# Kernel optimization log

Measured on AMD Instinct MI355X. Metric: run time of the kernel, lower is better.

The kernel has to match this reference:

```python
import jax, jax.numpy as jnp
import numpy as np
from jax.ops import segment_sum, segment_max

N, H, E, NEXP, K, L, HEADS, NM = 384, 768, 12288, 8, 2, 3, 4, 38
GAMMA, LAMBDA_SPD = 2.0, 0.5


def _ln(x, g, b, eps=1e-5):
    m = jnp.mean(x, -1, keepdims=True)
    v = jnp.mean((x - m) ** 2, -1, keepdims=True)
    return (x - m) / jnp.sqrt(v + eps) * g + b


def _gelu(x):
    return jax.nn.gelu(x, approximate=False)


def setup_inputs() -> dict:
    key = jax.random.key(0)
    ks = jax.random.split(key, 20)
    r = lambda i, sh: jax.random.normal(ks[i], sh, jnp.float32) * 0.02
    z = lambda sh: jnp.zeros(sh, jnp.float32)
    o = lambda sh: jnp.ones(sh, jnp.float32)
    return dict(
        feat_text=jax.random.normal(ks[0], (N, H), jnp.float32),
        feat_image=jax.random.normal(ks[1], (N, H), jnp.float32),
        spd_matrix=jax.random.uniform(ks[2], (N, N), dtype=jnp.float32),
        src=jax.random.randint(ks[3], (E,), 0, N, jnp.int32),
        dst=jax.random.randint(ks[4], (E,), 0, N, jnp.int32),
        mask_idx=jax.random.randint(ks[5], (NM,), 0, N, jnp.int32),
        mask_token=r(6, (H,)),
        gate_W=r(7, (H, NEXP)), gate_b=z((NEXP,)),
        exp_W1=r(8, (NEXP, H, H)), exp_b1=z((NEXP, H)),
        exp_g1=o((NEXP, H)), exp_be1=z((NEXP, H)),
        exp_W2=r(9, (NEXP, H, H)), exp_b2=z((NEXP, H)),
        gat_W=r(10, (L, H, HEADS * H)), gat_al=r(11, (L, HEADS, H)),
        gat_ar=r(12, (L, HEADS, H)), gat_b=z((L, HEADS * H)),
        dec_W1=r(13, (2, H, H)), dec_b1=z((2, H)),
        dec_g=o((2, H)), dec_be=z((2, H)),
        dec_W2=r(14, (2, H, H)), dec_b2=z((2, H)),
        spd_W1=r(15, (2 * H, H)), spd_b1=z((H,)),
        spd_g=o((H,)), spd_be=z((H,)),
        spd_W2=r(16, (H, 1)), spd_b2=z((1,)),
    )


def _forward(feat_text, feat_image, spd_matrix, mask_token, gate_W, gate_b,
             exp_W1, exp_b1, exp_g1, exp_be1, exp_W2, exp_b2,
             gat_W, gat_al, gat_ar, gat_b,
             dec_W1, dec_b1, dec_g, dec_be, dec_W2, dec_b2,
             spd_W1, spd_b1, spd_g, spd_be, spd_W2, spd_b2,
             src, dst, mask_idx):
    # mean of domain features, then mask-token replacement at fixed indices
    x = (feat_text + feat_image) * 0.5
    xm = x.at[mask_idx].set(mask_token)

    # --- MoE (all experts computed densely, top-2 gathered, as in source) ---
    gw = jax.nn.softmax(xm @ gate_W + gate_b, axis=-1)              # [N,NEXP]
    topw, topi = jax.lax.top_k(gw, K)
    topw = topw / jnp.sum(topw, -1, keepdims=True)
    eh = _gelu(_ln(jnp.einsum('nd,edh->neh', xm, exp_W1) + exp_b1, exp_g1, exp_be1))
    eo = jnp.einsum('neh,ehk->nek', eh, exp_W2) + exp_b2            # [N,NEXP,H]
    sel = jnp.take_along_axis(eo, topi[:, :, None], axis=1)          # [N,K,H]
    h = jnp.sum(sel * topw[:, :, None], axis=1)                      # [N,H]

    # --- stacked GATConv layers (DGL semantics), head-mean after each ---
    for l in range(L):
        f = (h @ gat_W[l]).reshape(N, HEADS, H)                      # [N,heads,H]
        el = jnp.sum(f * gat_al[l], -1)                              # [N,heads]
        er = jnp.sum(f * gat_ar[l], -1)
        e = jax.nn.leaky_relu(el[src] + er[dst], 0.2)                # [E,heads]
        emax = segment_max(e, dst, num_segments=N)
        emax = jnp.where(jnp.isfinite(emax), emax, 0.0)
        ex = jnp.exp(e - emax[dst])
        den = segment_sum(ex, dst, num_segments=N)
        alpha = ex / jnp.maximum(den[dst], 1e-9)                     # edge softmax by dst
        rst = segment_sum(alpha[:, :, None] * f[src], dst, num_segments=N)
        h = jnp.mean(rst + gat_b[l].reshape(HEADS, H), axis=1)       # [N,H]

    # --- domain reconstruction loss on masked nodes ---
    hm = h[mask_idx]
    feats = (feat_text, feat_image)
    recon = jnp.float32(0.0)
    for d in range(2):
        zz = _gelu(_ln(hm @ dec_W1[d] + dec_b1[d], dec_g[d], dec_be[d]))
        rec = zz @ dec_W2[d] + dec_b2[d]
        orig = feats[d][mask_idx]
        denom = jnp.maximum(jnp.linalg.norm(rec, axis=-1) * jnp.linalg.norm(orig, axis=-1), 1e-8)
        cos = jnp.sum(rec * orig, -1) / denom
        recon = recon + jnp.mean((1.0 - cos) ** GAMMA)

    # --- SPD loss over all N^2 pairs, vectorized ---
    # concat([h_i, h_j]) @ W1 == h_i @ W1[:H] + h_j @ W1[H:]  (exact decomposition)
    pa = h @ spd_W1[:H]                                              # [N,H]
    pb = h @ spd_W1[H:]                                              # [N,H]
    zp = _gelu(_ln(pa[:, None, :] + pb[None, :, :] + spd_b1, spd_g, spd_be))  # [N,N,H]
    pred = (zp @ spd_W2)[..., 0] + spd_b2[0]                         # [N,N]
    spd_loss = jnp.mean((pred - spd_matrix) ** 2)

    total = recon + LAMBDA_SPD * spd_loss
    return total, h


def reference(feat_text, feat_image, spd_matrix, src, dst, mask_idx, mask_token,
              gate_W, gate_b, exp_W1, exp_b1, exp_g1, exp_be1, exp_W2, exp_b2,
              gat_W, gat_al, gat_ar, gat_b,
              dec_W1, dec_b1, dec_g, dec_be, dec_W2, dec_b2,
              spd_W1, spd_b1, spd_g, spd_be, spd_W2, spd_b2):
    return _forward(feat_text, feat_image, spd_matrix, mask_token, gate_W, gate_b,
                    exp_W1, exp_b1, exp_g1, exp_be1, exp_W2, exp_b2,
                    gat_W, gat_al, gat_ar, gat_b,
                    dec_W1, dec_b1, dec_g, dec_be, dec_W2, dec_b2,
                    spd_W1, spd_b1, spd_g, spd_be, spd_W2, spd_b2,
                    src, dst, mask_idx)
```

## Files before the change

kernel.cpp:

```cpp
#include <hip/hip_runtime.h>
#include <hip/hip_bf16.h>
#include <math.h>

#define NN 384
#define HD 768
#define EE 12288
#define NCHUNK (EE / 256)
#define NEXPERT 8
#define TOPK 2
#define NLAYER 3
#define NHEADS 4
#define NMASK 38

typedef __attribute__((ext_vector_type(8))) short short8v;
typedef __attribute__((ext_vector_type(4))) float f32x4;
typedef __attribute__((ext_vector_type(2))) float f32x2;
typedef __attribute__((ext_vector_type(4))) int int4v;

__device__ __forceinline__ float gelu_f(float x) {
    return x * 0.5f * (1.f + erff(x * 0.70710678118654752440f));
}

__device__ __forceinline__ ushort f2bf(float x) {
    unsigned u = __float_as_uint(x);
    u += 0x7fffu + ((u >> 16) & 1u);
    return (ushort)(u >> 16);
}

__global__ __launch_bounds__(256) void k_xm_gate(const float* __restrict__ a,
        const float* __restrict__ b, const int* __restrict__ mask_idx,
        const float* __restrict__ mt, ushort* __restrict__ xm_bf,
        const float* __restrict__ gW, const float* __restrict__ gb,
        int* __restrict__ topi, float* __restrict__ topw) {
    int n = blockIdx.x, tid = threadIdx.x;
    __shared__ float xs[HD];
    __shared__ int ism;
    __shared__ float logits[NEXPERT];
    if (tid == 0) ism = 0;
    __syncthreads();
    if (tid < NMASK && mask_idx[tid] == n) ism = 1;
    __syncthreads();
#pragma unroll
    for (int r = 0; r < 3; r++) {
        int j = r * 256 + tid;
        float v = ism ? mt[j] : 0.5f * (a[(size_t)n * HD + j] + b[(size_t)n * HD + j]);
        xs[j] = v;
        xm_bf[(size_t)n * HD + j] = f2bf(v);
    }
// ... 23 lines not shown
        for (int e = 0; e < NEXPERT; e++) if (e != i0 && sm[e] > b1v) { b1v = sm[e]; i1 = e; }
        float ssum = b0 + b1v;
        topi[n * 2] = i0; topi[n * 2 + 1] = i1;
        topw[n * 2] = b0 / ssum; topw[n * 2 + 1] = b1v / ssum;
    }
}

__global__ __launch_bounds__(256) void k_transpose_all(
        const float* __restrict__ w1, const float* __restrict__ w2,
        const float* __restrict__ gw, const float* __restrict__ sw,
        const float* __restrict__ dw1, const float* __restrict__ dw2,
        ushort* __restrict__ o1, ushort* __restrict__ o2, ushort* __restrict__ og,
        ushort* __restrict__ os, ushort* __restrict__ od1, ushort* __restrict__ od2) {
    int b = blockIdx.x;
    const float* src; ushort* dst; int N, loc, tilesX;
    if (b < 4608)       { src = w1;  dst = o1;  N = HD;     loc = b;         tilesX = 24; }
    else if (b < 9216)  { src = w2;  dst = o2;  N = HD;     loc = b - 4608;  tilesX = 24; }
    else if (b < 16128) { src = gw;  dst = og;  N = 4 * HD; loc = b - 9216;  tilesX = 96; }
    else if (b < 17280) { src = sw;  dst = os;  N = HD;     loc = b - 16128; tilesX = 24; }
    else if (b < 18432) { src = dw1; dst = od1; N = HD;     loc = b - 17280; tilesX = 24; }
    else                { src = dw2; dst = od2; N = HD;     loc = b - 18432; tilesX = 24; }
    const int K = HD;
    int tilesPerZ = tilesX * 24;
    int z = loc / tilesPerZ;
    int rem = loc - z * tilesPerZ;
    int ty = rem / tilesX, tx = rem - ty * tilesX;
    const float* inz = src + (size_t)z * K * N;
    ushort* outz = dst + (size_t)z * K * N;
    int n0 = tx * 32, k0 = ty * 32;

    __shared__ float t[32][36];
    int r = threadIdx.x >> 3, c4 = (threadIdx.x & 7) * 4;
    float4 v = *reinterpret_cast<const float4*>(inz + (size_t)(k0 + r) * N + n0 + c4);
    t[r][c4] = v.x; t[r][c4 + 1] = v.y; t[r][c4 + 2] = v.z; t[r][c4 + 3] = v.w;
    __syncthreads();
    int orow = n0 + r;
    uint2 p;
    ushort b0 = f2bf(t[c4 + 0][r]);
    ushort b1 = f2bf(t[c4 + 1][r]);
    ushort b2 = f2bf(t[c4 + 2][r]);
    ushort b3 = f2bf(t[c4 + 3][r]);
    p.x = (unsigned)b0 | ((unsigned)b1 << 16);
    p.y = (unsigned)b2 | ((unsigned)b3 << 16);
    *reinterpret_cast<uint2*>(outz + (size_t)orow * K + k0 + c4) = p;
}

__global__ __launch_bounds__(256) void k_moe_meta(const int* __restrict__ topi,
        int* __restrict__ ecnt, int* __restrict__ estart, int* __restrict__ posArr,
        int* __restrict__ eofpos, int* __restrict__ rowlist, int* __restrict__ dec_rs) {
    __shared__ int ti[NN * TOPK];
    __shared__ int cnt[NEXPERT];
    __shared__ int est[NEXPERT + 1];
    int tid = threadIdx.x;
    if (tid < NEXPERT) cnt[tid] = 0;
    __syncthreads();
    for (int a = tid; a < NN * TOPK; a += 256) ti[a] = topi[a];
    __syncthreads();
    for (int a = tid; a < NN * TOPK; a += 256) atomicAdd(&cnt[ti[a]], 1);
    __syncthreads();
    if (tid == 0) {
        int s = 0;
        for (int e = 0; e < NEXPERT; e++) { est[e] = s; s += cnt[e]; }
        est[NEXPERT] = s;
        dec_rs[0] = 0; dec_rs[1] = NMASK;
    }
    __syncthreads();
    if (tid < NEXPERT) { ecnt[tid] = cnt[tid]; estart[tid] = est[tid]; }
    if (tid == 0) estart[NEXPERT] = est[NEXPERT];
    for (int a = tid; a < NN * TOPK; a += 256) {
        int e = ti[a]; int rank = 0;
        for (int a2 = 0; a2 < a; a2++) rank += (ti[a2] == e) ? 1 : 0;
        int p = est[e] + rank;
        posArr[a] = p; eofpos[p] = e; rowlist[p] = a >> 1;
    }
}

__global__ __launch_bounds__(256) void k_hist(const int* __restrict__ dst,
                                              int* __restrict__ counts) {
    __shared__ int h[NN];
    int c = blockIdx.x;
    for (int i = threadIdx.x; i < NN; i += 256) h[i] = 0;
    __syncthreads();
    atomicAdd(&h[dst[c * 256 + threadIdx.x]], 1);
    __syncthreads();
    for (int i = threadIdx.x; i < NN; i += 256) counts[c * NN + i] = h[i];
}

__global__ __launch_bounds__(NN) void k_scan_all(const int* __restrict__ counts,
        int* __restrict__ chunkbase, int* __restrict__ nstart) {
    __shared__ int tot[NN];
    int n = threadIdx.x;
    int s = 0;
    for (int c = 0; c < NCHUNK; c++) { chunkbase[c * NN + n] = s; s += counts[c * NN + n]; }
    tot[n] = s;
    __syncthreads();
    for (int off = 1; off < NN; off <<= 1) {
        int v = tot[n];
        int add = (n >= off) ? tot[n - off] : 0;
        __syncthreads();
        tot[n] = v + add;
        __syncthreads();
    }
    nstart[n + 1] = tot[n];
    if (n == 0) nstart[0] = 0;
}

__global__ __launch_bounds__(256) void k_rank2(const int* __restrict__ dst,
        const int* __restrict__ chunkbase, const int* __restrict__ nstart,
        int* __restrict__ esorted) {
    __shared__ int ds[256];
    int c = blockIdx.x;
    int e = c * 256 + threadIdx.x;
    int d = dst[e];
    ds[threadIdx.x] = d;
    __syncthreads();
    int r = 0;
    for (int i = 0; i < threadIdx.x; i++) r += (ds[i] == d) ? 1 : 0;
    esorted[nstart[d] + chunkbase[c * NN + d] + r] = e;
}

__device__ __forceinline__ short8v ldfrag(const ushort* s, int r, int kb) {
    int c = kb ^ (r & 7);
    return *reinterpret_cast<const short8v*>(s + r * 64 + c * 8);
}

__global__ __launch_bounds__(256) void k_mfma_gemm(
        const ushort* __restrict__ A, const ushort* __restrict__ Bt, float* __restrict__ C,
        int M, int K, int lda, int ldc, long strideBt, long strideC,
        const int* __restrict__ rowsA, const int* __restrict__ Ms,
        const int* __restrict__ rowStarts) {
    int z = blockIdx.z;
    int Meff = Ms ? Ms[z] : M;
    int row0 = blockIdx.y * 64;
    if (row0 >= Meff) return;
    int col0 = blockIdx.x * 64;
    int rowbase = rowStarts ? rowStarts[z] : 0;
    const ushort* Btz = Bt + (size_t)z * strideBt;
    float* Cz = C + (size_t)rowbase * ldc + (size_t)z * strideC;
    const int* rz = rowsA ? (rowsA + rowbase) : nullptr;

    __shared__ ushort Asm[64 * 64];
    __shared__ ushort Bsm[64 * 64];

    int tid = threadIdx.x;
    int w = tid >> 6, lane = tid & 63;
    int wr = w >> 1, wc = w & 1;
    int l15 = lane & 15, lq = lane >> 4;

    f32x4 acc[2][2];
#pragma unroll
    for (int i = 0; i < 2; i++)
#pragma unroll
        for (int j = 0; j < 2; j++) acc[i][j] = (f32x4){0.f, 0.f, 0.f, 0.f};

    for (int k0 = 0; k0 < K; k0 += 64) {
#pragma unroll
        for (int ii = 0; ii < 2; ii++) {
// ... 25 lines not shown
        }
        __syncthreads();
    }
#pragma unroll
    for (int ai = 0; ai < 2; ai++)
#pragma unroll
        for (int bi = 0; bi < 2; bi++) {
            int rbase = row0 + wr * 32 + ai * 16 + (lq << 2);
            int cc = col0 + wc * 32 + bi * 16 + l15;
#pragma unroll
            for (int r = 0; r < 4; r++) {
                int rr = rbase + r;
                if (rr < Meff) Cz[(size_t)rr * ldc + cc] = acc[ai][bi][r];
            }
        }
}

__global__ __launch_bounds__(256) void k_ln_gelu(const float* __restrict__ t1,
        ushort* __restrict__ ehb, const float* __restrict__ b1, const float* __restrict__ g,
        const float* __restrict__ be, const int* __restrict__ eofpos) {
    int row = blockIdx.x;
    int e = eofpos[row];
    int tid = threadIdx.x;
    __shared__ float rA[4], rB[4];
    float v[3]; float s1 = 0.f, s2 = 0.f;
#pragma unroll
    for (int r = 0; r < 3; r++) {
        int c = r * 256 + tid;
        float x = t1[(size_t)row * HD + c] + b1[e * HD + c];
        v[r] = x; s1 += x; s2 += x * x;
// ... 141 lines not shown
        }
        __syncthreads();
    }
#pragma unroll
    for (int r = 0; r < 3; r++) {
        int j = r * 256 + tid;
        float s = 0.f;
#pragma unroll
        for (int hd = 0; hd < NHEADS; hd++) s += acc[hd][r] + gb[hd * HD + j];
        float hv = 0.25f * s;
        hout[(size_t)n * HD + j] = hv;
        hb[(size_t)n * HD + j] = f2bf(hv);
    }
}

__global__ __launch_bounds__(256) void k_ln_gelu_dec(const float* __restrict__ t1,
        ushort* __restrict__ zzb, const float* __restrict__ b1, const float* __restrict__ g,
        const float* __restrict__ be) {
    int m = blockIdx.x, d = blockIdx.y;
    int row = d * NMASK + m;
    int tid = threadIdx.x;
    __shared__ float rA[4], rB[4];
    float v[3]; float s1 = 0.f, s2 = 0.f;
#pragma unroll
    for (int r = 0; r < 3; r++) {
        int c = r * 256 + tid;
        float x = t1[(size_t)row * HD + c] + b1[d * HD + c];
        v[r] = x; s1 += x; s2 += x * x;
    }
#pragma unroll
    for (int mm = 1; mm < 64; mm <<= 1) { s1 += __shfl_xor(s1, mm); s2 += __shfl_xor(s2, mm); }
    int wave = tid >> 6, lane = tid & 63;
    if (lane == 0) { rA[wave] = s1; rB[wave] = s2; }
    __syncthreads();
    float S1 = rA[0] + rA[1] + rA[2] + rA[3];
    float S2 = rB[0] + rB[1] + rB[2] + rB[3];
    float mean = S1 * (1.f / HD);
    float var = S2 * (1.f / HD) - mean * mean;
    float rstd = rsqrtf(var + 1e-5f);
#pragma unroll
    for (int r = 0; r < 3; r++) {
        int c = r * 256 + tid;
        float zn = (v[r] - mean) * rstd * g[d * HD + c] + be[d * HD + c];
        zzb[(size_t)row * HD + c] = f2bf(gelu_f(zn));
    }
}

__global__ __launch_bounds__(256) void k_cos(const float* __restrict__ rec,
        const float* __restrict__ b2, const int* __restrict__ mask_idx,
        const float* __restrict__ ft, const float* __restrict__ fi,
        float* __restrict__ rec_part) {
    int b = blockIdx.x;
    int d = b / NMASK, m = b % NMASK;
    int node = mask_idx[m];
    int tid = threadIdx.x;
    __shared__ float rA[4], rB[4], rC[4];
    const float* rrow = rec + (size_t)b * HD;
    const float* orig = (d == 0 ? ft : fi) + (size_t)node * HD;
    float pro = 0.f, prr = 0.f, poo = 0.f;
#pragma unroll
    for (int r = 0; r < 3; r++) {
        int c = r * 256 + tid;
        float rv = rrow[c] + b2[d * HD + c];
        float o = orig[c];
        pro += rv * o; prr += rv * rv; poo += o * o;
    }
#pragma unroll
    for (int mm = 1; mm < 64; mm <<= 1) {
        pro += __shfl_xor(pro, mm); prr += __shfl_xor(prr, mm); poo += __shfl_xor(poo, mm);
    }
    int wave = tid >> 6, lane = tid & 63;
    if (lane == 0) { rA[wave] = pro; rB[wave] = prr; rC[wave] = poo; }
    __syncthreads();
    if (tid == 0) {
        float P = rA[0] + rA[1] + rA[2] + rA[3];
        float R = rB[0] + rB[1] + rB[2] + rB[3];
        float O = rC[0] + rC[1] + rC[2] + rC[3];
        float denom = fmaxf(sqrtf(R) * sqrtf(O), 1e-8f);
        float cosv = P / denom;
        float t = 1.f - cosv;
        rec_part[b] = (t * t) * (1.f / (float)NMASK);
    }
}

__global__ __launch_bounds__(256) void k_spd_prep(float* __restrict__ pab,
        const float* __restrict__ b1, ushort* __restrict__ pp_bf,
        float* __restrict__ Svec, float* __restrict__ Qvec) {
    int r = blockIdx.x, tid = threadIdx.x;
    bool isA = r < NN;
    float* row = pab + (size_t)r * HD;
    __shared__ float rA[4], rB[4];
    float vv[3]; float s1 = 0.f, s2 = 0.f;
#pragma unroll
    for (int rr = 0; rr < 3; rr++) {
        int j = rr * 256 + tid;
        float v = row[j];
        if (isA) v += b1[j];
        vv[rr] = v; s1 += v; s2 += v * v;
    }
#pragma unroll
    for (int m = 1; m < 64; m <<= 1) { s1 += __shfl_xor(s1, m); s2 += __shfl_xor(s2, m); }
    int wave = tid >> 6, lane = tid & 63;
    if (lane == 0) { rA[wave] = s1; rB[wave] = s2; }
#pragma unroll
    for (int rr = 0; rr < 3; rr++) {
        int j = rr * 256 + tid;
        if (isA) row[j] = vv[rr];
        pp_bf[(size_t)r * HD + j] = f2bf(vv[rr]);
    }
    __syncthreads();
    if (tid == 0) {
        Svec[r] = rA[0] + rA[1] + rA[2] + rA[3];
        Qvec[r] = rB[0] + rB[1] + rB[2] + rB[3];
    }
}

#define GC1 2.3022085f
#define GC2 0.10294429f
__global__ __launch_bounds__(256) void k_spd2(const float* __restrict__ pab,
        const float* __restrict__ Svec, const float* __restrict__ Qvec,
        const float* __restrict__ cross, const float* __restrict__ g,
        const float* __restrict__ be, const float* __restrict__ w2,
        const float* __restrict__ b2, const float* __restrict__ spd,
        float* __restrict__ partials) {
    __shared__ float wsum[4];
    int i = blockIdx.x;
    int wave = threadIdx.x >> 6, lane = threadIdx.x & 63;
    const f32x2* paP = reinterpret_cast<const f32x2*>(pab + (size_t)i * HD);
    const f32x2* gP = reinterpret_cast<const f32x2*>(g);
    const f32x2* beP = reinterpret_cast<const f32x2*>(be);
    const f32x2* w2P = reinterpret_cast<const f32x2*>(w2);
    f32x2 pa2[6], g2[6], be2[6], w22[6];
#pragma unroll
    for (int r = 0; r < 6; r++) {
        int e = r * 64 + lane;
        pa2[r] = paP[e];
        g2[r] = gP[e];
        be2[r] = beP[e];
        w22[r] = w2P[e];
    }
    float Sa = Svec[i], Qa = Qvec[i];
    float bacc = 0.f;
    float b2v = b2[0];
    for (int j = blockIdx.y * 4 + wave; j < NN; j += 32) {
        const f32x2* pbj = reinterpret_cast<const f32x2*>(pab + (size_t)(NN + j) * HD);
        float mean = (Sa + Svec[NN + j]) * (1.f / HD);
        float ex2 = (Qa + Qvec[NN + j] + 2.f * cross[(size_t)i * NN + j]) * (1.f / HD);
        float var = ex2 - mean * mean;
        float rstd = rsqrtf(var + 1e-5f);
        f32x2 rstd2 = (f32x2){rstd, rstd};
        float nmr = -mean * rstd;
        f32x2 nmr2 = (f32x2){nmr, nmr};
        f32x2 dot2 = (f32x2){0.f, 0.f};
#pragma unroll
        for (int r = 0; r < 6; r++) {
            f32x2 z = pa2[r] + pbj[r * 64 + lane];
            f32x2 u = z * rstd2 + nmr2;
            f32x2 zn = u * g2[r] + be2[r];
            f32x2 t2 = zn * zn;
            f32x2 p = t2 * (f32x2){GC2, GC2} + (f32x2){GC1, GC1};
            f32x2 ua = zn * p;
            float e0 = __builtin_amdgcn_exp2f(-ua.x);
            float e1 = __builtin_amdgcn_exp2f(-ua.y);
            f32x2 rr = (f32x2){__builtin_amdgcn_rcpf(1.f + e0),
                               __builtin_amdgcn_rcpf(1.f + e1)};
            f32x2 gl = zn * rr;
            dot2 = gl * w22[r] + dot2;
        }
        float dot = dot2.x + dot2.y;
#pragma unroll
        for (int m = 1; m < 64; m <<= 1) dot += __shfl_xor(dot, m);
        if (lane == 0) {
            float d = (dot + b2v) - spd[(size_t)i * NN + j];
            bacc += d * d;
        }
    }
    if (lane == 0) wsum[wave] = bacc;
    __syncthreads();
    if (threadIdx.x == 0) partials[i * 8 + blockIdx.y] = wsum[0] + wsum[1] + wsum[2] + wsum[3];
}

__global__ __launch_bounds__(256) void k_out(const float* __restrict__ h,
        const float* __restrict__ rec_part, const float* __restrict__ spd_part,
        float* __restrict__ out) {
    if (blockIdx.x < NN * HD / 256) {
        int i = blockIdx.x * 256 + threadIdx.x;
        out[1 + i] = h[i];
        return;
    }
    __shared__ float rA[4], rB[4];
    int tid = threadIdx.x;
    float sp = 0.f, rc = 0.f;
    for (int t = tid; t < 8 * NN; t += 256) sp += spd_part[t];
    for (int t = tid; t < 2 * NMASK; t += 256) rc += rec_part[t];
#pragma unroll
    for (int m = 1; m < 64; m <<= 1) { sp += __shfl_xor(sp, m); rc += __shfl_xor(rc, m); }
    int wave = tid >> 6, lane = tid & 63;
    if (lane == 0) { rA[wave] = sp; rB[wave] = rc; }
    __syncthreads();
    if (tid == 0) {
        float SP = rA[0] + rA[1] + rA[2] + rA[3];
        float RC = rB[0] + rB[1] + rB[2] + rB[3];
        out[0] = RC + 0.5f * (SP * (1.f / ((float)NN * (float)NN)));
    }
}

extern "C" void kernel_launch(void* const* d_in, const int* in_sizes, int n_in,
                              void* d_out, int out_size, void* d_ws, size_t ws_size,
// ... 35 lines not shown
    size_t off = 0;
    auto alloc = [&](size_t nfl) { float* p = ws + off; off += (nfl + 3) & ~(size_t)3; return p; };
    float* hA   = alloc((size_t)NN * HD);
    float* hB   = alloc((size_t)NN * HD);
    float* t1   = alloc((size_t)NN * TOPK * HD);
    float* eo   = alloc((size_t)NN * TOPK * HD);
    float* fbuf = alloc((size_t)NN * NHEADS * HD);
    float* el   = alloc(NN * NHEADS);
    float* er   = alloc(NN * NHEADS);
    float* pab  = alloc((size_t)2 * NN * HD);
    float* cross = alloc((size_t)NN * NN);
    float* Svec = alloc(2 * NN);
    float* Qvec = alloc(2 * NN);
    float* topw = alloc(NN * TOPK);
    float* rec_part = alloc(2 * NMASK + 4);
    float* spd_part = alloc(8 * NN);
    int* topi    = (int*)alloc(NN * TOPK);
    int* ecnt    = (int*)alloc(16);
    int* estart  = (int*)alloc(16);
    int* posArr  = (int*)alloc(NN * TOPK);
    int* eofpos  = (int*)alloc(NN * TOPK);
    int* rowlist = (int*)alloc(NN * TOPK);
    int* dec_rs  = (int*)alloc(4);
    int* nstart  = (int*)alloc(NN + 4);
    int* esorted = (int*)alloc(EE);
    int* counts    = (int*)alloc((size_t)NCHUNK * NN);
    int* chunkbase = (int*)alloc((size_t)NCHUNK * NN);
    ushort* xm_bf  = (ushort*)alloc((size_t)NN * HD / 2);
    ushort* eh_bf  = (ushort*)alloc((size_t)NN * TOPK * HD / 2);
    ushort* hA_bf  = (ushort*)alloc((size_t)NN * HD / 2);
    ushort* hB_bf  = (ushort*)alloc((size_t)NN * HD / 2);
    ushort* pp_bf  = (ushort*)alloc((size_t)2 * NN * HD / 2);
    ushort* expW1t = (ushort*)alloc((size_t)NEXPERT * HD * HD / 2);
    ushort* expW2t = (ushort*)alloc((size_t)NEXPERT * HD * HD / 2);
    ushort* gatWt  = (ushort*)alloc((size_t)NLAYER * NHEADS * HD * HD / 2);
    ushort* spdW1t = (ushort*)alloc((size_t)2 * HD * HD / 2);
    ushort* decW1t = (ushort*)alloc((size_t)2 * HD * HD / 2);
    ushort* decW2t = (ushort*)alloc((size_t)2 * HD * HD / 2);

    k_transpose_all<<<dim3(19584), dim3(256), 0, stream>>>(
        exp_W1, exp_W2, gat_W, spd_W1, dec_W1, dec_W2,
        expW1t, expW2t, gatWt, spdW1t, decW1t, decW2t);

    k_xm_gate<<<dim3(NN), dim3(256), 0, stream>>>(
        feat_text, feat_image, mask_idx, mask_token, xm_bf, gate_W, gate_b, topi, topw);
    k_moe_meta<<<dim3(1), dim3(256), 0, stream>>>(topi, ecnt, estart, posArr, eofpos,
                                                  rowlist, dec_rs);

    k_hist<<<dim3(NCHUNK), dim3(256), 0, stream>>>(dst, counts);
    k_scan_all<<<dim3(1), dim3(NN), 0, stream>>>(counts, chunkbase, nstart);
    k_rank2<<<dim3(NCHUNK), dim3(256), 0, stream>>>(dst, chunkbase, nstart, esorted);

    k_mfma_gemm<<<dim3(HD / 64, 12, NEXPERT), dim3(256), 0, stream>>>(
        xm_bf, expW1t, t1, 0, HD, HD, HD, (long)HD * HD, 0, rowlist, ecnt, estart);
    k_ln_gelu<<<dim3(NN * TOPK), dim3(256), 0, stream>>>(t1, eh_bf, exp_b1, exp_g1, exp_be1, eofpos);
    k_mfma_gemm<<<dim3(HD / 64, 12, NEXPERT), dim3(256), 0, stream>>>(
        eh_bf, expW2t, eo, 0, HD, HD, HD, (long)HD * HD, 0, nullptr, ecnt, estart);
    k_combine_moe<<<dim3(NN), dim3(256), 0, stream>>>(eo, exp_b2, topi, topw, posArr, hA, hA_bf);

    float* hcur = hA; float* hnxt = hB;
    ushort* hcur_bf = hA_bf; ushort* hnxt_bf = hB_bf;
    for (int l = 0; l < NLAYER; l++) {
        k_mfma_gemm<<<dim3(NHEADS * HD / 64, NN / 64, 1), dim3(256), 0, stream>>>(
            hcur_bf, gatWt + (size_t)l * NHEADS * HD * HD, fbuf,
            NN, HD, HD, NHEADS * HD, 0, 0, nullptr, nullptr, nullptr);
        k_el_er<<<dim3(NN), dim3(256), 0, stream>>>(
            fbuf, gat_al + (size_t)l * NHEADS * HD, gat_ar + (size_t)l * NHEADS * HD, el, er);
        k_gat_agg<<<dim3(NN), dim3(256), 0, stream>>>(
            fbuf, el, er, src, esorted, nstart, gat_b + (size_t)l * NHEADS * HD, hnxt, hnxt_bf);
        float* t = hcur; hcur = hnxt; hnxt = t;
        ushort* tb = hcur_bf; hcur_bf = hnxt_bf; hnxt_bf = tb;
    }

    k_mfma_gemm<<<dim3(HD / 64, 1, 2), dim3(256), 0, stream>>>(
        hcur_bf, decW1t, t1, NMASK, HD, HD, HD, (long)HD * HD, (long)NMASK * HD,
        mask_idx, nullptr, nullptr);
    k_ln_gelu_dec<<<dim3(NMASK, 2), dim3(256), 0, stream>>>(t1, eh_bf, dec_b1, dec_g, dec_be);
    k_mfma_gemm<<<dim3(HD / 64, 1, 2), dim3(256), 0, stream>>>(
        eh_bf, decW2t, eo, NMASK, HD, HD, HD, (long)HD * HD, 0,
        nullptr, nullptr, dec_rs);
    k_cos<<<dim3(2 * NMASK), dim3(256), 0, stream>>>(
        eo, dec_b2, mask_idx, feat_text, feat_image, rec_part);

    k_mfma_gemm<<<dim3(HD / 64, NN / 64, 2), dim3(256), 0, stream>>>(
        hcur_bf, spdW1t, pab, NN, HD, HD, HD, (long)HD * HD, (long)NN * HD,
        nullptr, nullptr, nullptr);
    k_spd_prep<<<dim3(2 * NN), dim3(256), 0, stream>>>(pab, spd_b1, pp_bf, Svec, Qvec);
    k_mfma_gemm<<<dim3(NN / 64, NN / 64, 1), dim3(256), 0, stream>>>(
        pp_bf, pp_bf + (size_t)NN * HD, cross, NN, HD, HD, NN, 0, 0,
        nullptr, nullptr, nullptr);
    k_spd2<<<dim3(NN, 8), dim3(256), 0, stream>>>(
        pab, Svec, Qvec, cross, spd_g, spd_be, spd_W2, spd_b2, spd_matrix, spd_part);

    k_out<<<dim3(NN * HD / 256 + 1), dim3(256), 0, stream>>>(
        hcur, rec_part, spd_part, (float*)d_out);
}
```

Before: 364.8 us.

## Merge independent small kernels into combined launches and retile transpose and SPD loop

Folds the edge histogram into the gate kernel, the scan and MoE metadata into one launch, and pairs the independent decoder and SPD GEMMs into dual-GEMM launches indexed by blockIdx.z. The decoder LN/GELU is merged into the SPD prep, and the cosine loss is merged into the SPD loss kernel. The goal is fewer serialized launches and better GPU fill during the tail. The weight transpose now handles 64x32 tiles with 16-byte stores, and the SPD loop is restructured to process two columns per iteration with 32 partials per row. In exchange, the kernels become more branchy and some blocks in the merged grids exit early as idle.

```diff
diff --git a/kernel.cpp b/kernel.cpp
--- a/kernel.cpp
+++ b/kernel.cpp
@@ -27,11 +27,22 @@
     return (ushort)(u >> 16);
 }
 
-__global__ __launch_bounds__(256) void k_xm_gate(const float* __restrict__ a,
+__global__ __launch_bounds__(256) void k_xm_gate_hist(const float* __restrict__ a,
         const float* __restrict__ b, const int* __restrict__ mask_idx,
         const float* __restrict__ mt, ushort* __restrict__ xm_bf,
         const float* __restrict__ gW, const float* __restrict__ gb,
-        int* __restrict__ topi, float* __restrict__ topw) {
+        int* __restrict__ topi, float* __restrict__ topw,
+        const int* __restrict__ dst, int* __restrict__ counts) {
+    if (blockIdx.x >= NN) {
+        __shared__ int h[NN];
+        int c = blockIdx.x - NN;
+        for (int i = threadIdx.x; i < NN; i += 256) h[i] = 0;
+        __syncthreads();
+        atomicAdd(&h[dst[c * 256 + threadIdx.x]], 1);
+        __syncthreads();
+        for (int i = threadIdx.x; i < NN; i += 256) counts[c * NN + i] = h[i];
+        return;
+    }
     int n = blockIdx.x, tid = threadIdx.x;
     __shared__ float xs[HD];
     __shared__ int ism;
@@ -85,49 +96,75 @@
         ushort* __restrict__ os, ushort* __restrict__ od1, ushort* __restrict__ od2) {
     int b = blockIdx.x;
     const float* src; ushort* dst; int N, loc, tilesX;
-    if (b < 4608)       { src = w1;  dst = o1;  N = HD;     loc = b;         tilesX = 24; }
-    else if (b < 9216)  { src = w2;  dst = o2;  N = HD;     loc = b - 4608;  tilesX = 24; }
-    else if (b < 16128) { src = gw;  dst = og;  N = 4 * HD; loc = b - 9216;  tilesX = 96; }
-    else if (b < 17280) { src = sw;  dst = os;  N = HD;     loc = b - 16128; tilesX = 24; }
-    else if (b < 18432) { src = dw1; dst = od1; N = HD;     loc = b - 17280; tilesX = 24; }
-    else                { src = dw2; dst = od2; N = HD;     loc = b - 18432; tilesX = 24; }
+    if (b < 2304)      { src = w1;  dst = o1;  N = HD;     loc = b;        tilesX = 24; }
+    else if (b < 4608) { src = w2;  dst = o2;  N = HD;     loc = b - 2304; tilesX = 24; }
+    else if (b < 8064) { src = gw;  dst = og;  N = 4 * HD; loc = b - 4608; tilesX = 96; }
+    else if (b < 8640) { src = sw;  dst = os;  N = HD;     loc = b - 8064; tilesX = 24; }
+    else if (b < 9216) { src = dw1; dst = od1; N = HD;     loc = b - 8640; tilesX = 24; }
+    else               { src = dw2; dst = od2; N = HD;     loc = b - 9216; tilesX = 24; }
     const int K = HD;
-    int tilesPerZ = tilesX * 24;
+    int tilesPerZ = tilesX * 12;
     int z = loc / tilesPerZ;
     int rem = loc - z * tilesPerZ;
     int ty = rem / tilesX, tx = rem - ty * tilesX;
     const float* inz = src + (size_t)z * K * N;
     ushort* outz = dst + (size_t)z * K * N;
-    int n0 = tx * 32, k0 = ty * 32;
-
-    __shared__ float t[32][36];
-    int r = threadIdx.x >> 3, c4 = (threadIdx.x & 7) * 4;
-    float4 v = *reinterpret_cast<const float4*>(inz + (size_t)(k0 + r) * N + n0 + c4);
-    t[r][c4] = v.x; t[r][c4 + 1] = v.y; t[r][c4 + 2] = v.z; t[r][c4 + 3] = v.w;
-    __syncthreads();
-    int orow = n0 + r;
-    uint2 p;
-    ushort b0 = f2bf(t[c4 + 0][r]);
-    ushort b1 = f2bf(t[c4 + 1][r]);
-    ushort b2 = f2bf(t[c4 + 2][r]);
-    ushort b3 = f2bf(t[c4 + 3][r]);
-    p.x = (unsigned)b0 | ((unsigned)b1 << 16);
-    p.y = (unsigned)b2 | ((unsigned)b3 << 16);
-    *reinterpret_cast<uint2*>(outz + (size_t)orow * K + k0 + c4) = p;
-}
-
-__global__ __launch_bounds__(256) void k_moe_meta(const int* __restrict__ topi,
-        int* __restrict__ ecnt, int* __restrict__ estart, int* __restrict__ posArr,
-        int* __restrict__ eofpos, int* __restrict__ rowlist, int* __restrict__ dec_rs) {
+    int n0 = tx * 32, k0 = ty * 64;
+
+    __shared__ float t[64][33];
+    int r = threadIdx.x >> 2, c8 = (threadIdx.x & 3) * 8;
+    const float* ip = inz + (size_t)(k0 + r) * N + n0 + c8;
+    float4 va = *reinterpret_cast<const float4*>(ip);
+    float4 vb = *reinterpret_cast<const float4*>(ip + 4);
+    t[r][c8 + 0] = va.x; t[r][c8 + 1] = va.y; t[r][c8 + 2] = va.z; t[r][c8 + 3] = va.w;
+    t[r][c8 + 4] = vb.x; t[r][c8 + 5] = vb.y; t[r][c8 + 6] = vb.z; t[r][c8 + 7] = vb.w;
+    __syncthreads();
+    int nn = threadIdx.x >> 3;
+    int kk = (threadIdx.x & 7) * 8;
+    uint4 o;
+    uint pk[4];
+#pragma unroll
+    for (int q = 0; q < 4; q++) {
+        ushort lo = f2bf(t[kk + 2 * q][nn]);
+        ushort hi = f2bf(t[kk + 2 * q + 1][nn]);
+        pk[q] = (uint)lo | ((uint)hi << 16);
+    }
+    o.x = pk[0]; o.y = pk[1]; o.z = pk[2]; o.w = pk[3];
+    *reinterpret_cast<uint4*>(outz + (size_t)(n0 + nn) * K + k0 + kk) = o;
+}
+
+__global__ __launch_bounds__(NN) void k_scan_meta(const int* __restrict__ counts,
+        int* __restrict__ chunkbase, int* __restrict__ nstart,
+        const int* __restrict__ topi, int* __restrict__ ecnt, int* __restrict__ estart,
+        int* __restrict__ posArr, int* __restrict__ eofpos, int* __restrict__ rowlist,
+        int* __restrict__ dec_rs) {
+    int tid = threadIdx.x;
+    if (blockIdx.x == 0) {
+        __shared__ int tot[NN];
+        int n = tid;
+        int s = 0;
+        for (int c = 0; c < NCHUNK; c++) { chunkbase[c * NN + n] = s; s += counts[c * NN + n]; }
+        tot[n] = s;
+        __syncthreads();
+        for (int off = 1; off < NN; off <<= 1) {
+            int v = tot[n];
+            int add = (n >= off) ? tot[n - off] : 0;
+            __syncthreads();
+            tot[n] = v + add;
+            __syncthreads();
+        }
+        nstart[n + 1] = tot[n];
+        if (n == 0) nstart[0] = 0;
+        return;
+    }
     __shared__ int ti[NN * TOPK];
     __shared__ int cnt[NEXPERT];
     __shared__ int est[NEXPERT + 1];
-    int tid = threadIdx.x;
     if (tid < NEXPERT) cnt[tid] = 0;
     __syncthreads();
-    for (int a = tid; a < NN * TOPK; a += 256) ti[a] = topi[a];
-    __syncthreads();
-    for (int a = tid; a < NN * TOPK; a += 256) atomicAdd(&cnt[ti[a]], 1);
+    for (int a = tid; a < NN * TOPK; a += NN) ti[a] = topi[a];
+    __syncthreads();
+    for (int a = tid; a < NN * TOPK; a += NN) atomicAdd(&cnt[ti[a]], 1);
     __syncthreads();
     if (tid == 0) {
         int s = 0;
@@ -138,42 +175,12 @@
     __syncthreads();
     if (tid < NEXPERT) { ecnt[tid] = cnt[tid]; estart[tid] = est[tid]; }
     if (tid == 0) estart[NEXPERT] = est[NEXPERT];
-    for (int a = tid; a < NN * TOPK; a += 256) {
+    for (int a = tid; a < NN * TOPK; a += NN) {
         int e = ti[a]; int rank = 0;
         for (int a2 = 0; a2 < a; a2++) rank += (ti[a2] == e) ? 1 : 0;
         int p = est[e] + rank;
         posArr[a] = p; eofpos[p] = e; rowlist[p] = a >> 1;
     }
-}
-
-__global__ __launch_bounds__(256) void k_hist(const int* __restrict__ dst,
-                                              int* __restrict__ counts) {
-    __shared__ int h[NN];
-    int c = blockIdx.x;
-    for (int i = threadIdx.x; i < NN; i += 256) h[i] = 0;
-    __syncthreads();
-    atomicAdd(&h[dst[c * 256 + threadIdx.x]], 1);
-    __syncthreads();
-    for (int i = threadIdx.x; i < NN; i += 256) counts[c * NN + i] = h[i];
-}
-
-__global__ __launch_bounds__(NN) void k_scan_all(const int* __restrict__ counts,
-        int* __restrict__ chunkbase, int* __restrict__ nstart) {
-    __shared__ int tot[NN];
-    int n = threadIdx.x;
-    int s = 0;
-    for (int c = 0; c < NCHUNK; c++) { chunkbase[c * NN + n] = s; s += counts[c * NN + n]; }
-    tot[n] = s;
-    __syncthreads();
-    for (int off = 1; off < NN; off <<= 1) {
-        int v = tot[n];
-        int add = (n >= off) ? tot[n - off] : 0;
-        __syncthreads();
-        tot[n] = v + add;
-        __syncthreads();
-    }
-    nstart[n + 1] = tot[n];
-    if (n == 0) nstart[0] = 0;
 }
 
 __global__ __launch_bounds__(256) void k_rank2(const int* __restrict__ dst,
@@ -195,23 +202,20 @@
     return *reinterpret_cast<const short8v*>(s + r * 64 + c * 8);
 }
 
-__global__ __launch_bounds__(256) void k_mfma_gemm(
+__device__ __forceinline__ void gemm_body(
         const ushort* __restrict__ A, const ushort* __restrict__ Bt, float* __restrict__ C,
-        int M, int K, int lda, int ldc, long strideBt, long strideC,
+        int M, int Ncol, int K, int lda, int ldc, long strideBt, long strideC,
         const int* __restrict__ rowsA, const int* __restrict__ Ms,
-        const int* __restrict__ rowStarts) {
-    int z = blockIdx.z;
+        const int* __restrict__ rowStarts, int z, ushort* Asm, ushort* Bsm) {
     int Meff = Ms ? Ms[z] : M;
     int row0 = blockIdx.y * 64;
     if (row0 >= Meff) return;
     int col0 = blockIdx.x * 64;
+    if (col0 >= Ncol) return;
     int rowbase = rowStarts ? rowStarts[z] : 0;
     const ushort* Btz = Bt + (size_t)z * strideBt;
     float* Cz = C + (size_t)rowbase * ldc + (size_t)z * strideC;
     const int* rz = rowsA ? (rowsA + rowbase) : nullptr;
-
-    __shared__ ushort Asm[64 * 64];
-    __shared__ ushort Bsm[64 * 64];
 
     int tid = threadIdx.x;
     int w = tid >> 6, lane = tid & 63;
@@ -267,6 +271,35 @@
                 if (rr < Meff) Cz[(size_t)rr * ldc + cc] = acc[ai][bi][r];
             }
         }
+}
+
+__global__ __launch_bounds__(256) void k_mfma_gemm(
+        const ushort* __restrict__ A, const ushort* __restrict__ Bt, float* __restrict__ C,
+        int M, int Ncol, int K, int lda, int ldc, long strideBt, long strideC,
+        const int* __restrict__ rowsA, const int* __restrict__ Ms,
+        const int* __restrict__ rowStarts) {
+    __shared__ ushort Asm[64 * 64];
+    __shared__ ushort Bsm[64 * 64];
+    gemm_body(A, Bt, C, M, Ncol, K, lda, ldc, strideBt, strideC, rowsA, Ms, rowStarts,
+              blockIdx.z, Asm, Bsm);
+}
+
+__global__ __launch_bounds__(256) void k_mfma_dual(
+        const ushort* __restrict__ A0, const ushort* __restrict__ Bt0, float* __restrict__ C0,
+        int M0, int Nc0, int lda0, int ldc0, long sBt0, long sC0,
+        const int* __restrict__ rows0, const int* __restrict__ rs0, int nz0,
+        const ushort* __restrict__ A1, const ushort* __restrict__ Bt1, float* __restrict__ C1,
+        int M1, int Nc1, int lda1, int ldc1, long sBt1, long sC1,
+        const int* __restrict__ rows1, const int* __restrict__ rs1) {
+    __shared__ ushort Asm[64 * 64];
+    __shared__ ushort Bsm[64 * 64];
+    int z = blockIdx.z;
+    if (z < nz0)
+        gemm_body(A0, Bt0, C0, M0, Nc0, HD, lda0, ldc0, sBt0, sC0, rows0, nullptr, rs0,
+                  z, Asm, Bsm);
+    else
+        gemm_body(A1, Bt1, C1, M1, Nc1, HD, lda1, ldc1, sBt1, sC1, rows1, nullptr, rs1,
+                  z - nz0, Asm, Bsm);
 }
 
 __global__ __launch_bounds__(256) void k_ln_gelu(const float* __restrict__ t1,
@@ -438,82 +471,45 @@
     }
 }
 
-__global__ __launch_bounds__(256) void k_ln_gelu_dec(const float* __restrict__ t1,
-        ushort* __restrict__ zzb, const float* __restrict__ b1, const float* __restrict__ g,
-        const float* __restrict__ be) {
-    int m = blockIdx.x, d = blockIdx.y;
-    int row = d * NMASK + m;
+__global__ __launch_bounds__(256) void k_lndec_prep(float* __restrict__ pab,
+        const float* __restrict__ b1, ushort* __restrict__ pp_bf,
+        float* __restrict__ Svec, float* __restrict__ Qvec,
+        const float* __restrict__ t1, ushort* __restrict__ zzb,
+        const float* __restrict__ db1, const float* __restrict__ dg,
+        const float* __restrict__ dbe) {
     int tid = threadIdx.x;
+    int wave = tid >> 6, lane = tid & 63;
     __shared__ float rA[4], rB[4];
-    float v[3]; float s1 = 0.f, s2 = 0.f;
-#pragma unroll
-    for (int r = 0; r < 3; r++) {
-        int c = r * 256 + tid;
-        float x = t1[(size_t)row * HD + c] + b1[d * HD + c];
-        v[r] = x; s1 += x; s2 += x * x;
-    }
-#pragma unroll
-    for (int mm = 1; mm < 64; mm <<= 1) { s1 += __shfl_xor(s1, mm); s2 += __shfl_xor(s2, mm); }
-    int wave = tid >> 6, lane = tid & 63;
-    if (lane == 0) { rA[wave] = s1; rB[wave] = s2; }
-    __syncthreads();
-    float S1 = rA[0] + rA[1] + rA[2] + rA[3];
-    float S2 = rB[0] + rB[1] + rB[2] + rB[3];
-    float mean = S1 * (1.f / HD);
-    float var = S2 * (1.f / HD) - mean * mean;
-    float rstd = rsqrtf(var + 1e-5f);
-#pragma unroll
-    for (int r = 0; r < 3; r++) {
-        int c = r * 256 + tid;
-        float zn = (v[r] - mean) * rstd * g[d * HD + c] + be[d * HD + c];
-        zzb[(size_t)row * HD + c] = f2bf(gelu_f(zn));
-    }
-}
-
-__global__ __launch_bounds__(256) void k_cos(const float* __restrict__ rec,
-        const float* __restrict__ b2, const int* __restrict__ mask_idx,
-        const float* __restrict__ ft, const float* __restrict__ fi,
-        float* __restrict__ rec_part) {
-    int b = blockIdx.x;
-    int d = b / NMASK, m = b % NMASK;
-    int node = mask_idx[m];
-    int tid = threadIdx.x;
-    __shared__ float rA[4], rB[4], rC[4];
-    const float* rrow = rec + (size_t)b * HD;
-    const float* orig = (d == 0 ? ft : fi) + (size_t)node * HD;
-    float pro = 0.f, prr = 0.f, poo = 0.f;
-#pragma unroll
-    for (int r = 0; r < 3; r++) {
-        int c = r * 256 + tid;
-        float rv = rrow[c] + b2[d * HD + c];
-        float o = orig[c];
-        pro += rv * o; prr += rv * rv; poo += o * o;
-    }
-#pragma unroll
-    for (int mm = 1; mm < 64; mm <<= 1) {
-        pro += __shfl_xor(pro, mm); prr += __shfl_xor(prr, mm); poo += __shfl_xor(poo, mm);
-    }
-    int wave = tid >> 6, lane = tid & 63;
-    if (lane == 0) { rA[wave] = pro; rB[wave] = prr; rC[wave] = poo; }
-    __syncthreads();
-    if (tid == 0) {
-        float P = rA[0] + rA[1] + rA[2] + rA[3];
-        float R = rB[0] + rB[1] + rB[2] + rB[3];
-        float O = rC[0] + rC[1] + rC[2] + rC[3];
-        float denom = fmaxf(sqrtf(R) * sqrtf(O), 1e-8f);
-        float cosv = P / denom;
-        float t = 1.f - cosv;
-        rec_part[b] = (t * t) * (1.f / (float)NMASK);
-    }
-}
-
-__global__ __launch_bounds__(256) void k_spd_prep(float* __restrict__ pab,
-        const float* __restrict__ b1, ushort* __restrict__ pp_bf,
-        float* __restrict__ Svec, float* __restrict__ Qvec) {
-    int r = blockIdx.x, tid = threadIdx.x;
+    if (blockIdx.x >= 2 * NN) {
+        int row = blockIdx.x - 2 * NN;
+        int d = row / NMASK;
+        float v[3]; float s1 = 0.f, s2 = 0.f;
+#pragma unroll
+        for (int r = 0; r < 3; r++) {
+            int c = r * 256 + tid;
+            float x = t1[(size_t)row * HD + c] + db1[d * HD + c];
+            v[r] = x; s1 += x; s2 += x * x;
+        }
+#pragma unroll
+        for (int mm = 1; mm < 64; mm <<= 1) { s1 += __shfl_xor(s1, mm); s2 += __shfl_xor(s2, mm); }
+        if (lane == 0) { rA[wave] = s1; rB[wave] = s2; }
+        __syncthreads();
+        float S1 = rA[0] + rA[1] + rA[2] + rA[3];
+        float S2 = rB[0] + rB[1] + rB[2] + rB[3];
+        float mean = S1 * (1.f / HD);
+        float var = S2 * (1.f / HD) - mean * mean;
+        float rstd = rsqrtf(var + 1e-5f);
+#pragma unroll
+        for (int r = 0; r < 3; r++) {
+            int c = r * 256 + tid;
+            float zn = (v[r] - mean) * rstd * dg[d * HD + c] + dbe[d * HD + c];
+            zzb[(size_t)row * HD + c] = f2bf(gelu_f(zn));
+        }
+        return;
+    }
+    int r = blockIdx.x;
     bool isA = r < NN;
     float* row = pab + (size_t)r * HD;
-    __shared__ float rA[4], rB[4];
     float vv[3]; float s1 = 0.f, s2 = 0.f;
 #pragma unroll
     for (int rr = 0; rr < 3; rr++) {
@@ -524,7 +520,6 @@
     }
 #pragma unroll
     for (int m = 1; m < 64; m <<= 1) { s1 += __shfl_xor(s1, m); s2 += __shfl_xor(s2, m); }
-    int wave = tid >> 6, lane = tid & 63;
     if (lane == 0) { rA[wave] = s1; rB[wave] = s2; }
 #pragma unroll
     for (int rr = 0; rr < 3; rr++) {
@@ -546,62 +541,125 @@
         const float* __restrict__ cross, const float* __restrict__ g,
         const float* __restrict__ be, const float* __restrict__ w2,
         const float* __restrict__ b2, const float* __restrict__ spd,
-        float* __restrict__ partials) {
-    __shared__ float wsum[4];
+        float* __restrict__ partials,
+        const float* __restrict__ rec, const float* __restrict__ db2,
+        const int* __restrict__ mask_idx, const float* __restrict__ ft,
+        const float* __restrict__ fi, float* __restrict__ rec_part) {
+    int wv = threadIdx.x >> 6, lane = threadIdx.x & 63;
+    if (blockIdx.y == 8) {
+        int b = blockIdx.x;
+        if (b >= 2 * NMASK) return;
+        int d = b / NMASK, m = b % NMASK;
+        int node = mask_idx[m];
+        int tid = threadIdx.x;
+        __shared__ float rA[4], rB[4], rC[4];
+        const float* rrow = rec + (size_t)b * HD;
+        const float* orig = (d == 0 ? ft : fi) + (size_t)node * HD;
+        float pro = 0.f, prr = 0.f, poo = 0.f;
+#pragma unroll
+        for (int r = 0; r < 3; r++) {
+            int c = r * 256 + tid;
+            float rv = rrow[c] + db2[d * HD + c];
+            float o = orig[c];
+            pro += rv * o; prr += rv * rv; poo += o * o;
+        }
+#pragma unroll
+        for (int mm = 1; mm < 64; mm <<= 1) {
+            pro += __shfl_xor(pro, mm); prr += __shfl_xor(prr, mm); poo += __shfl_xor(poo, mm);
+        }
+        if (lane == 0) { rA[wv] = pro; rB[wv] = prr; rC[wv] = poo; }
+        __syncthreads();
+        if (tid == 0) {
+            float P = rA[0] + rA[1] + rA[2] + rA[3];
+            float R = rB[0] + rB[1] + rB[2] + rB[3];
+            float O = rC[0] + rC[1] + rC[2] + rC[3];
+            float denom = fmaxf(sqrtf(R) * sqrtf(O), 1e-8f);
+            float cosv = P / denom;
+            float t = 1.f - cosv;
+            rec_part[b] = (t * t) * (1.f / (float)NMASK);
+        }
+        return;
+    }
     int i = blockIdx.x;
-    int wave = threadIdx.x >> 6, lane = threadIdx.x & 63;
-    const f32x2* paP = reinterpret_cast<const f32x2*>(pab + (size_t)i * HD);
-    const f32x2* gP = reinterpret_cast<const f32x2*>(g);
-    const f32x2* beP = reinterpret_cast<const f32x2*>(be);
-    const f32x2* w2P = reinterpret_cast<const f32x2*>(w2);
+    int y = blockIdx.y * 4 + wv;
+    const f32x2* paP = reinterpret_cast<const f32x2*>(pab + (size_t)i * HD) + lane;
+    const f32x2* gP  = reinterpret_cast<const f32x2*>(g) + lane;
+    const f32x2* beP = reinterpret_cast<const f32x2*>(be) + lane;
+    const f32x2* wP  = reinterpret_cast<const f32x2*>(w2) + lane;
     f32x2 pa2[6], g2[6], be2[6], w22[6];
 #pragma unroll
-    for (int r = 0; r < 6; r++) {
-        int e = r * 64 + lane;
-        pa2[r] = paP[e];
-        g2[r] = gP[e];
-        be2[r] = beP[e];
-        w22[r] = w2P[e];
-    }
+    for (int s = 0; s < 6; s++) {
+        pa2[s] = paP[s * 64];
+        g2[s]  = gP[s * 64];
+        be2[s] = beP[s * 64];
+        w22[s] = wP[s * 64];
+    }
+#pragma unroll
+    for (int s = 0; s < 6; s++) {
+        asm volatile("" : "+v"(pa2[s]), "+v"(g2[s]), "+v"(be2[s]), "+v"(w22[s]));
+    }
+    const f32x2 C1v = (f32x2){GC1, GC1};
+    const f32x2 C2v = (f32x2){GC2, GC2};
+    const f32x2 one2 = (f32x2){1.f, 1.f};
     float Sa = Svec[i], Qa = Qvec[i];
+    float b2v = b2[0];
     float bacc = 0.f;
-    float b2v = b2[0];
-    for (int j = blockIdx.y * 4 + wave; j < NN; j += 32) {
-        const f32x2* pbj = reinterpret_cast<const f32x2*>(pab + (size_t)(NN + j) * HD);
-        float mean = (Sa + Svec[NN + j]) * (1.f / HD);
-        float ex2 = (Qa + Qvec[NN + j] + 2.f * cross[(size_t)i * NN + j]) * (1.f / HD);
-        float var = ex2 - mean * mean;
-        float rstd = rsqrtf(var + 1e-5f);
-        f32x2 rstd2 = (f32x2){rstd, rstd};
-        float nmr = -mean * rstd;
-        f32x2 nmr2 = (f32x2){nmr, nmr};
-        f32x2 dot2 = (f32x2){0.f, 0.f};
-#pragma unroll
-        for (int r = 0; r < 6; r++) {
-            f32x2 z = pa2[r] + pbj[r * 64 + lane];
-            f32x2 u = z * rstd2 + nmr2;
-            f32x2 zn = u * g2[r] + be2[r];
-            f32x2 t2 = zn * zn;
-            f32x2 p = t2 * (f32x2){GC2, GC2} + (f32x2){GC1, GC1};
-            f32x2 ua = zn * p;
-            float e0 = __builtin_amdgcn_exp2f(-ua.x);
-            float e1 = __builtin_amdgcn_exp2f(-ua.y);
-            f32x2 rr = (f32x2){__builtin_amdgcn_rcpf(1.f + e0),
-                               __builtin_amdgcn_rcpf(1.f + e1)};
-            f32x2 gl = zn * rr;
-            dot2 = gl * w22[r] + dot2;
-        }
-        float dot = dot2.x + dot2.y;
-#pragma unroll
-        for (int m = 1; m < 64; m <<= 1) dot += __shfl_xor(dot, m);
+#pragma unroll
+    for (int t = 0; t < 6; t++) {
+        int ja = y + (2 * t) * 32;
+        int jb = y + (2 * t + 1) * 32;
+        const f32x2* pA = reinterpret_cast<const f32x2*>(pab + (size_t)(NN + ja) * HD) + lane;
+        const f32x2* pB = reinterpret_cast<const f32x2*>(pab + (size_t)(NN + jb) * HD) + lane;
+        float meanA = (Sa + Svec[NN + ja]) * (1.f / HD);
+        float exA = (Qa + Qvec[NN + ja] + 2.f * cross[(size_t)i * NN + ja]) * (1.f / HD);
+        float rsA = rsqrtf(exA - meanA * meanA + 1e-5f);
+        float nmA = -meanA * rsA;
+        float meanB = (Sa + Svec[NN + jb]) * (1.f / HD);
+        float exB = (Qa + Qvec[NN + jb] + 2.f * cross[(size_t)i * NN + jb]) * (1.f / HD);
+        float rsB = rsqrtf(exB - meanB * meanB + 1e-5f);
+        float nmB = -meanB * rsB;
+        f32x2 rsA2 = (f32x2){rsA, rsA}, nmA2 = (f32x2){nmA, nmA};
+        f32x2 rsB2 = (f32x2){rsB, rsB}, nmB2 = (f32x2){nmB, nmB};
+        f32x2 dA = (f32x2){0.f, 0.f}, dB = (f32x2){0.f, 0.f};
+#pragma unroll
+        for (int s = 0; s < 6; s++) {
+            f32x2 zA = pa2[s] + pA[s * 64];
+            f32x2 zB = pa2[s] + pB[s * 64];
+            f32x2 znA = (zA * rsA2 + nmA2) * g2[s] + be2[s];
+            f32x2 znB = (zB * rsB2 + nmB2) * g2[s] + be2[s];
+            f32x2 uaA = znA * (znA * znA * C2v + C1v);
+            f32x2 uaB = znB * (znB * znB * C2v + C1v);
+            f32x2 eA, eB;
+            eA.x = __builtin_amdgcn_exp2f(-uaA.x);
+            eA.y = __builtin_amdgcn_exp2f(-uaA.y);
+            eB.x = __builtin_amdgcn_exp2f(-uaB.x);
+            eB.y = __builtin_amdgcn_exp2f(-uaB.y);
+            f32x2 qA = eA + one2;
+            f32x2 qB = eB + one2;
+            f32x2 rrA, rrB;
+            rrA.x = __builtin_amdgcn_rcpf(qA.x);
+            rrA.y = __builtin_amdgcn_rcpf(qA.y);
+            rrB.x = __builtin_amdgcn_rcpf(qB.x);
+            rrB.y = __builtin_amdgcn_rcpf(qB.y);
+            f32x2 nwA = znA * w22[s];
+            f32x2 nwB = znB * w22[s];
+            dA = nwA * rrA + dA;
+            dB = nwB * rrB + dB;
+        }
+        float dotA = dA.x + dA.y;
+        float dotB = dB.x + dB.y;
+#pragma unroll
+        for (int m = 1; m < 64; m <<= 1) {
+            dotA += __shfl_xor(dotA, m);
+            dotB += __shfl_xor(dotB, m);
+        }
         if (lane == 0) {
-            float d = (dot + b2v) - spd[(size_t)i * NN + j];
-            bacc += d * d;
-        }
-    }
-    if (lane == 0) wsum[wave] = bacc;
-    __syncthreads();
-    if (threadIdx.x == 0) partials[i * 8 + blockIdx.y] = wsum[0] + wsum[1] + wsum[2] + wsum[3];
+            float da = (dotA + b2v) - spd[(size_t)i * NN + ja];
+            float db = (dotB + b2v) - spd[(size_t)i * NN + jb];
+            bacc += da * da + db * db;
+        }
+    }
+    if (lane == 0) partials[i * 32 + y] = bacc;
 }
 
 __global__ __launch_bounds__(256) void k_out(const float* __restrict__ h,
@@ -615,7 +673,7 @@
     __shared__ float rA[4], rB[4];
     int tid = threadIdx.x;
     float sp = 0.f, rc = 0.f;
-    for (int t = tid; t < 8 * NN; t += 256) sp += spd_part[t];
+    for (int t = tid; t < 32 * NN; t += 256) sp += spd_part[t];
     for (int t = tid; t < 2 * NMASK; t += 256) rc += rec_part[t];
 #pragma unroll
     for (int m = 1; m < 64; m <<= 1) { sp += __shfl_xor(sp, m); rc += __shfl_xor(rc, m); }
@@ -681,7 +739,7 @@
     float* Qvec = alloc(2 * NN);
     float* topw = alloc(NN * TOPK);
     float* rec_part = alloc(2 * NMASK + 4);
-    float* spd_part = alloc(8 * NN);
+    float* spd_part = alloc(32 * NN);
     int* topi    = (int*)alloc(NN * TOPK);
     int* ecnt    = (int*)alloc(16);
     int* estart  = (int*)alloc(16);
@@ -705,24 +763,23 @@
     ushort* decW1t = (ushort*)alloc((size_t)2 * HD * HD / 2);
     ushort* decW2t = (ushort*)alloc((size_t)2 * HD * HD / 2);
 
-    k_transpose_all<<<dim3(19584), dim3(256), 0, stream>>>(
+    k_transpose_all<<<dim3(9792), dim3(256), 0, stream>>>(
         exp_W1, exp_W2, gat_W, spd_W1, dec_W1, dec_W2,
         expW1t, expW2t, gatWt, spdW1t, decW1t, decW2t);
 
-    k_xm_gate<<<dim3(NN), dim3(256), 0, stream>>>(
-        feat_text, feat_image, mask_idx, mask_token, xm_bf, gate_W, gate_b, topi, topw);
-    k_moe_meta<<<dim3(1), dim3(256), 0, stream>>>(topi, ecnt, estart, posArr, eofpos,
-                                                  rowlist, dec_rs);
-
-    k_hist<<<dim3(NCHUNK), dim3(256), 0, stream>>>(dst, counts);
-    k_scan_all<<<dim3(1), dim3(NN), 0, stream>>>(counts, chunkbase, nstart);
+    k_xm_gate_hist<<<dim3(NN + NCHUNK), dim3(256), 0, stream>>>(
+        feat_text, feat_image, mask_idx, mask_token, xm_bf, gate_W, gate_b, topi, topw,
+        dst, counts);
+
+    k_scan_meta<<<dim3(2), dim3(NN), 0, stream>>>(
+        counts, chunkbase, nstart, topi, ecnt, estart, posArr, eofpos, rowlist, dec_rs);
     k_rank2<<<dim3(NCHUNK), dim3(256), 0, stream>>>(dst, chunkbase, nstart, esorted);
 
     k_mfma_gemm<<<dim3(HD / 64, 12, NEXPERT), dim3(256), 0, stream>>>(
-        xm_bf, expW1t, t1, 0, HD, HD, HD, (long)HD * HD, 0, rowlist, ecnt, estart);
+        xm_bf, expW1t, t1, 0, HD, HD, HD, HD, (long)HD * HD, 0, rowlist, ecnt, estart);
     k_ln_gelu<<<dim3(NN * TOPK), dim3(256), 0, stream>>>(t1, eh_bf, exp_b1, exp_g1, exp_be1, eofpos);
     k_mfma_gemm<<<dim3(HD / 64, 12, NEXPERT), dim3(256), 0, stream>>>(
-        eh_bf, expW2t, eo, 0, HD, HD, HD, (long)HD * HD, 0, nullptr, ecnt, estart);
+        eh_bf, expW2t, eo, 0, HD, HD, HD, HD, (long)HD * HD, 0, nullptr, ecnt, estart);
     k_combine_moe<<<dim3(NN), dim3(256), 0, stream>>>(eo, exp_b2, topi, topw, posArr, hA, hA_bf);
 
     float* hcur = hA; float* hnxt = hB;
@@ -730,7 +787,7 @@
     for (int l = 0; l < NLAYER; l++) {
         k_mfma_gemm<<<dim3(NHEADS * HD / 64, NN / 64, 1), dim3(256), 0, stream>>>(
             hcur_bf, gatWt + (size_t)l * NHEADS * HD * HD, fbuf,
-            NN, HD, HD, NHEADS * HD, 0, 0, nullptr, nullptr, nullptr);
+            NN, NHEADS * HD, HD, HD, NHEADS * HD, 0, 0, nullptr, nullptr, nullptr);
         k_el_er<<<dim3(NN), dim3(256), 0, stream>>>(
             fbuf, gat_al + (size_t)l * NHEADS * HD, gat_ar + (size_t)l * NHEADS * HD, el, er);
         k_gat_agg<<<dim3(NN), dim3(256), 0, stream>>>(
@@ -739,25 +796,24 @@
         ushort* tb = hcur_bf; hcur_bf = hnxt_bf; hnxt_bf = tb;
     }
 
-    k_mfma_gemm<<<dim3(HD / 64, 1, 2), dim3(256), 0, stream>>>(
+    k_mfma_dual<<<dim3(HD / 64, NN / 64, 4), dim3(256), 0, stream>>>(
+        hcur_bf, spdW1t, pab, NN, HD, HD, HD, (long)HD * HD, (long)NN * HD,
+        nullptr, nullptr, 2,
         hcur_bf, decW1t, t1, NMASK, HD, HD, HD, (long)HD * HD, (long)NMASK * HD,
-        mask_idx, nullptr, nullptr);
-    k_ln_gelu_dec<<<dim3(NMASK, 2), dim3(256), 0, stream>>>(t1, eh_bf, dec_b1, dec_g, dec_be);
-    k_mfma_gemm<<<dim3(HD / 64, 1, 2), dim3(256), 0, stream>>>(
+        mask_idx, nullptr);
+
+    k_lndec_prep<<<dim3(2 * NN + 2 * NMASK), dim3(256), 0, stream>>>(
+        pab, spd_b1, pp_bf, Svec, Qvec, t1, eh_bf, dec_b1, dec_g, dec_be);
+
+    k_mfma_dual<<<dim3(HD / 64, NN / 64, 3), dim3(256), 0, stream>>>(
         eh_bf, decW2t, eo, NMASK, HD, HD, HD, (long)HD * HD, 0,
-        nullptr, nullptr, dec_rs);
-    k_cos<<<dim3(2 * NMASK), dim3(256), 0, stream>>>(
+        nullptr, dec_rs, 2,
+        pp_bf, pp_bf + (size_t)NN * HD, cross, NN, NN, HD, NN, 0, 0,
+        nullptr, nullptr);
+
+    k_spd2<<<dim3(NN, 9), dim3(256), 0, stream>>>(
+        pab, Svec, Qvec, cross, spd_g, spd_be, spd_W2, spd_b2, spd_matrix, spd_part,
         eo, dec_b2, mask_idx, feat_text, feat_image, rec_part);
-
-    k_mfma_gemm<<<dim3(HD / 64, NN / 64, 2), dim3(256), 0, stream>>>(
-        hcur_bf, spdW1t, pab, NN, HD, HD, HD, (long)HD * HD, (long)NN * HD,
-        nullptr, nullptr, nullptr);
-    k_spd_prep<<<dim3(2 * NN), dim3(256), 0, stream>>>(pab, spd_b1, pp_bf, Svec, Qvec);
-    k_mfma_gemm<<<dim3(NN / 64, NN / 64, 1), dim3(256), 0, stream>>>(
-        pp_bf, pp_bf + (size_t)NN * HD, cross, NN, HD, HD, NN, 0, 0,
-        nullptr, nullptr, nullptr);
-    k_spd2<<<dim3(NN, 8), dim3(256), 0, stream>>>(
-        pab, Svec, Qvec, cross, spd_g, spd_be, spd_W2, spd_b2, spd_matrix, spd_part);
 
     k_out<<<dim3(NN * HD / 256 + 1), dim3(256), 0, stream>>>(
         hcur, rec_part, spd_part, (float*)d_out);
```

Measured after the change: 322.0 us. -11.7%, faster.
